# Performance work log

Hardware: AMD Instinct MI355X
Metric: run time of the kernel (lower is better)

The kernel has to match this reference:

```python
import jax, jax.numpy as jnp
import numpy as np

NODES_PER_GRAPH = 57
NUM_BRANCHES = 80
NUM_GRAPHS = 4096
IN_CH = 4
HID = 128
NUM_LAYERS = 5
BN_EPS = 1e-5


def setup_inputs() -> dict:
    key = jax.random.key(0)
    ks = jax.random.split(key, 24)
    N = NUM_GRAPHS * NODES_PER_GRAPH
    E = NUM_GRAPHS * NUM_BRANCHES * 2  # bidirectional branches per graph
    x = jax.random.normal(ks[0], (N, IN_CH), dtype=jnp.float32)
    # within-graph random edges, offset per graph block
    ep = jax.random.randint(ks[1], (2, E), 0, NODES_PER_GRAPH, dtype=jnp.int32)
    off = jnp.repeat(jnp.arange(NUM_GRAPHS, dtype=jnp.int32) * NODES_PER_GRAPH,
                     NUM_BRANCHES * 2)
    edge_index = ep + off[None, :]
    i = np.arange(NUM_BRANCHES)
    branch_u = jnp.asarray(i % NODES_PER_GRAPH, dtype=jnp.int32)
    branch_v = jnp.asarray((i * 7 + 3) % NODES_PER_GRAPH, dtype=jnp.int32)
    s = 0.05
    return {
        "x": x, "edge_index": edge_index,
        "branch_u": branch_u, "branch_v": branch_v,
        "Wp": jax.random.normal(ks[2], (IN_CH, HID)) * s,
        "bp": jnp.zeros((HID,), jnp.float32),
        "conv_W": jax.random.normal(ks[3], (NUM_LAYERS, HID, HID)) * s,
        "conv_b": jnp.zeros((NUM_LAYERS, HID), jnp.float32),
        "bn_gamma": jnp.ones((NUM_LAYERS, HID), jnp.float32),
        "bn_beta": jnp.zeros((NUM_LAYERS, HID), jnp.float32),
        "bn_mean": jax.random.normal(ks[4], (NUM_LAYERS, HID)) * 0.1,
        "bn_var": jax.random.uniform(ks[5], (NUM_LAYERS, HID)) + 0.5,
        "phys_W1": jax.random.normal(ks[6], (HID, 16)) * s,
        "phys_b1": jnp.zeros((16,), jnp.float32),
        "phys_W2": jax.random.normal(ks[7], (16, 1)) * s,
        "phys_b2": jnp.zeros((1,), jnp.float32),
        "mlp_W1": jax.random.normal(ks[8], (2 * HID + 1, HID)) * s,
        "mlp_b1": jnp.zeros((HID,), jnp.float32),
        "mlp_W2": jax.random.normal(ks[9], (HID, 1)) * s,
        "mlp_b2": jnp.zeros((1,), jnp.float32),
    }


def _gcn_conv(x, edge_index, W, b, num_nodes):
    # PyG GCNConv: add self-loops, symmetric deg^{-1/2} normalization,
    # message = norm * (x @ W)[src], scatter-add into dst, then + bias.
    h = x @ W
    loop = jnp.arange(num_nodes, dtype=edge_index.dtype)
    src = jnp.concatenate([edge_index[0], loop])
    dst = jnp.concatenate([edge_index[1], loop])
    deg = jax.ops.segment_sum(jnp.ones_like(dst, dtype=h.dtype), dst,
                              num_segments=num_nodes)  # >= 1 (self-loop)
    dinv = jax.lax.rsqrt(deg)
    norm = dinv[src] * dinv[dst]  # [E+N]
    out = jax.ops.segment_sum(h[src] * norm[:, None], dst,
                              num_segments=num_nodes)
    return out + b


def _forward(x, edge_index, branch_u, branch_v, Wp, bp, conv_W, conv_b,
             bn_gamma, bn_beta, bn_mean, bn_var, phys_W1, phys_b1, phys_W2,
             phys_b2, mlp_W1, mlp_b1, mlp_W2, mlp_b2):
    N = x.shape[0]
    num_graphs = N // NODES_PER_GRAPH
    h = x @ Wp + bp
    for l in range(NUM_LAYERS):
        res = h
        h = _gcn_conv(h, edge_index, conv_W[l], conv_b[l], N)
        # BatchNorm1d in eval mode (running stats); dropout is identity in eval
        h = (h - bn_mean[l]) * jax.lax.rsqrt(bn_var[l] + BN_EPS) * bn_gamma[l] + bn_beta[l]
        h = jax.nn.relu(h)
        h = h + res
    theta = jax.nn.relu(h @ phys_W1 + phys_b1) @ phys_W2 + phys_b2  # [N,1]
    offsets = (jnp.arange(num_graphs, dtype=jnp.int32) * NODES_PER_GRAPH)
    u_idx = (branch_u[None, :] + offsets[:, None]).reshape(-1)
    v_idx = (branch_v[None, :] + offsets[:, None]).reshape(-1)
    edge_feat = jnp.concatenate([h[u_idx], h[v_idx]], axis=-1)  # [G*80, 2H]
    delta_theta = theta[u_idx] - theta[v_idx]                   # [G*80, 1]
    comb = jnp.concatenate([edge_feat, delta_theta], axis=-1)
    return jax.nn.relu(comb @ mlp_W1 + mlp_b1) @ mlp_W2 + mlp_b2


def reference(x, edge_index, branch_u, branch_v, Wp, bp, conv_W, conv_b,
              bn_gamma, bn_beta, bn_mean, bn_var, phys_W1, phys_b1, phys_W2,
              phys_b2, mlp_W1, mlp_b1, mlp_W2, mlp_b2):
    return _forward(x, edge_index, branch_u, branch_v, Wp, bp, conv_W, conv_b,
                    bn_gamma, bn_beta, bn_mean, bn_var, phys_W1, phys_b1,
                    phys_W2, phys_b2, mlp_W1, mlp_b1, mlp_W2, mlp_b2)
```

## Files before the change

### kernel.cpp

```cpp
#include <hip/hip_runtime.h>

#define NPG 57
#define NEPG 160
#define NB 80
#define HID 128
#define NG 4096
#define NL 5

typedef __attribute__((ext_vector_type(8))) short bf16x8;
typedef __attribute__((ext_vector_type(4))) float f32x4;

__device__ __forceinline__ short f2bf(float f) {
    unsigned u = __builtin_bit_cast(unsigned, f);
    u += 0x7fff + ((u >> 16) & 1);
    return (short)(u >> 16);
}
__device__ __forceinline__ float bf2f(short s) {
    unsigned u = ((unsigned)(unsigned short)s) << 16;
    return __builtin_bit_cast(float, u);
}

__device__ __forceinline__ void cvt_pack(float4 a, float4 b, bf16x8& h8, bf16x8& l8) {
#define CVT1(X, I) { short hj = f2bf(X); h8[I] = hj; l8[I] = f2bf((X) - bf2f(hj)); }
    CVT1(a.x, 0) CVT1(a.y, 1) CVT1(a.z, 2) CVT1(a.w, 3)
    CVT1(b.x, 4) CVT1(b.y, 5) CVT1(b.z, 6) CVT1(b.w, 7)
#undef CVT1
}

__device__ __forceinline__ void frag_ks(const float (*A)[HID], int row, int kb, int ks,
                                        bf16x8& fh, bf16x8& fl) {
    const int sw = (row & 7) << 2;
    const float* rp = A[row];
    float4 q0 = *(const float4*)&rp[(32 * ks + kb) ^ sw];
    float4 q1 = *(const float4*)&rp[(32 * ks + kb + 4) ^ sw];
    cvt_pack(q0, q1, fh, fl);
}

template<int NCT>
__device__ __forceinline__ void mm_ks(f32x4* acc, const bf16x8& fh, const bf16x8& fl,
                                      const short* __restrict__ whi,
                                      const short* __restrict__ wlo,
                                      int ln15, int kb, int ks, int ctbase) {
#pragma unroll
    for (int j = 0; j < NCT; ++j) {
        int ct = ctbase + j;
        bf16x8 bhi = *(const bf16x8*)(whi + (16 * ct + ln15) * HID + kb + 32 * ks);
        bf16x8 blo = *(const bf16x8*)(wlo + (16 * ct + ln15) * HID + kb + 32 * ks);
        f32x4 a = acc[j];
        a = __builtin_amdgcn_mfma_f32_16x16x32_bf16(fh, bhi, a, 0, 0, 0);
        a = __builtin_amdgcn_mfma_f32_16x16x32_bf16(fh, blo, a, 0, 0, 0);
        a = __builtin_amdgcn_mfma_f32_16x16x32_bf16(fl, bhi, a, 0, 0, 0);
        acc[j] = a;
    }
}

__global__ void prep(const float* __restrict__ convW, const float* __restrict__ mlpW1,
                     const float* __restrict__ physW1, const float* __restrict__ convb,
                     const float* __restrict__ bn_gamma, const float* __restrict__ bn_beta,
                     const float* __restrict__ bn_mean, const float* __restrict__ bn_var,
                     short* __restrict__ wb, float* __restrict__ fsc, float* __restrict__ fsh) {
    int id = blockIdx.x * 256 + threadIdx.x;
    if (id < 114688) {
        int mat = id >> 14, rem = id & 16383, n = rem >> 7, k = rem & 127;
        float w;
        if (mat < 5)       w = convW[mat * 16384 + k * 128 + n];
        else if (mat == 5) w = mlpW1[k * 128 + n];
        else               w = mlpW1[(128 + k) * 128 + n];
        short hi = f2bf(w);
        short lo = f2bf(w - bf2f(hi));
        wb[mat * 32768 + n * 128 + k] = hi;
        wb[mat * 32768 + 16384 + n * 128 + k] = lo;
    } else if (id < 116736) {
        int p = id - 114688, n = p >> 7, k = p & 127;
        float w = physW1[k * 16 + n];
        short hi = f2bf(w);
        short lo = f2bf(w - bf2f(hi));
        wb[229376 + p] = hi;
        wb[231424 + p] = lo;
    } else if (id < 117376) {
        int p = id - 116736;
        float sc = bn_gamma[p] * rsqrtf(bn_var[p] + 1e-5f);
        float sh = fmaf(convb[p] - bn_mean[p], sc, bn_beta[p]);
        fsc[p] = sc;
        fsh[p] = sh;
    }
}

__global__ __launch_bounds__(512, 2) void pinn_fused(
    const float* __restrict__ x, const int* __restrict__ edge_index,
    const int* __restrict__ branch_u, const int* __restrict__ branch_v,
    const float* __restrict__ Wp, const float* __restrict__ bp,
    const float* __restrict__ physb1, const float* __restrict__ physW2,
    const float* __restrict__ physb2,
    const float* __restrict__ mlpW1, const float* __restrict__ mlpb1,
    const float* __restrict__ mlpW2, const float* __restrict__ mlpb2,
    const short* __restrict__ wb, const float* __restrict__ fsc,
    const float* __restrict__ fsh, float* __restrict__ out) {
    __shared__ float h[64][HID];
    __shared__ float dinv[NPG];
    __shared__ int   deg[NPG];
    __shared__ int   rowptr[NPG + 1];
    __shared__ int   cursor[NPG];
    __shared__ short esrc[NEPG], edst[NEPG];
    __shared__ int2  csre[NEPG + NPG];
    __shared__ float theta[64];
    __shared__ float red[NB];
    __shared__ int   bu[NB], bv[NB];

    const int g = blockIdx.x;
    const int tid = threadIdx.x;
    const int lane = tid & 63;
    const int wv = tid >> 6;
    const int ln15 = lane & 15;
    const int hi4 = lane >> 4;
    const int kb = hi4 << 3;
    const int c = tid & 127;
    const int rg = tid >> 7;
    const int wrow = wv & 3;
    const int ctbase = (wv >> 2) * 4;
    const int row = 16 * wrow + ln15;
    const int r0 = 16 * wrow + 4 * hi4;

    {
        float w0 = Wp[c], w1 = Wp[HID + c], w2 = Wp[2 * HID + c], w3 = Wp[3 * HID + c];
        float bb = bp[c];
        for (int r = rg; r < NPG; r += 4) {
            float4 xv = ((const float4*)x)[g * NPG + r];
            h[r][c ^ ((r & 7) << 2)] =
                fmaf(xv.x, w0, fmaf(xv.y, w1, fmaf(xv.z, w2, fmaf(xv.w, w3, bb))));
        }
    }
    if (tid < NPG) deg[tid] = 1;
    if (tid < NB) { bu[tid] = branch_u[tid]; bv[tid] = branch_v[tid]; red[tid] = 0.f; }
    for (int i = tid; i < 7 * HID; i += 512) h[57 + (i >> 7)][i & 127] = 0.f;
    __syncthreads();

    if (tid < NEPG) {
        int gs = edge_index[g * NEPG + tid];
        int gd = edge_index[NG * NEPG + g * NEPG + tid];
        short ls = (short)(gs - g * NPG);
        short ld = (short)(gd - g * NPG);
        esrc[tid] = ls;
        edst[tid] = ld;
        atomicAdd(&deg[ld], 1);
    }
    __syncthreads();

    if (wv == 0) {
        int dv = (lane < NPG) ? deg[lane] : 0;
        if (lane < NPG) dinv[lane] = rsqrtf((float)dv);
        int val = dv;
#pragma unroll
        for (int o = 1; o < 64; o <<= 1) {
            int t = __shfl_up(val, o, 64);
            if (lane >= o) val += t;
        }
        if (lane < NPG) { rowptr[lane + 1] = val; cursor[lane] = val - dv; }
        if (lane == 0) rowptr[0] = 0;
    }
    __syncthreads();

    if (tid < NEPG) {
        int s = esrc[tid], d = edst[tid];
        int pos = atomicAdd(&cursor[d], 1);
        csre[pos] = make_int2(s, __builtin_bit_cast(int, dinv[s] * dinv[d]));
    }
    if (tid < NPG) {
        int pos = atomicAdd(&cursor[tid], 1);
        csre[pos] = make_int2(tid, __builtin_bit_cast(int, dinv[tid] * dinv[tid]));
    }
    __syncthreads();

    for (int l = 0; l < NL; ++l) {
        const short* whi = wb + 2 * l * 16384;
        const short* wlo = wb + (2 * l + 1) * 16384;
        const int e0 = (row < NPG) ? rowptr[row] : 0;
        const int e1 = (row < NPG) ? rowptr[row + 1] : 0;

        f32x4 acc[4];
#pragma unroll
        for (int j = 0; j < 4; ++j) acc[j] = (f32x4){0.f, 0.f, 0.f, 0.f};

#pragma unroll
        for (int ks = 0; ks < 4; ++ks) {
            float4 pa = {0.f, 0.f, 0.f, 0.f};
            float4 qa = {0.f, 0.f, 0.f, 0.f};
            for (int e = e0; e < e1; ++e) {
                int2 ce = csre[e];
                const float* hp = h[ce.x];
                float w = __builtin_bit_cast(float, ce.y);
                const int sw = (ce.x & 7) << 2;
                float4 p0 = *(const float4*)&hp[(32 * ks + kb) ^ sw];
                float4 p1 = *(const float4*)&hp[(32 * ks + kb + 4) ^ sw];
                pa.x = fmaf(w, p0.x, pa.x); pa.y = fmaf(w, p0.y, pa.y);
                pa.z = fmaf(w, p0.z, pa.z); pa.w = fmaf(w, p0.w, pa.w);
                qa.x = fmaf(w, p1.x, qa.x); qa.y = fmaf(w, p1.y, qa.y);
                qa.z = fmaf(w, p1.z, qa.z); qa.w = fmaf(w, p1.w, qa.w);
            }
            bf16x8 fh, fl;
            cvt_pack(pa, qa, fh, fl);
            mm_ks<4>(acc, fh, fl, whi, wlo, ln15, kb, ks, ctbase);
        }
        __syncthreads();

        const float* sc = fsc + l * HID;
        const float* sh = fsh + l * HID;
#pragma unroll
        for (int j = 0; j < 4; ++j) {
            int ch = 16 * (ctbase + j) + ln15;
            float scv = sc[ch], shv = sh[ch];
#pragma unroll
            for (int q = 0; q < 4; ++q) {
                int rr = r0 + q;
                if (rr < NPG) {
                    float v = fmaf(acc[j][q], scv, shv);
                    int idx = ch ^ ((rr & 7) << 2);
                    h[rr][idx] = fmaxf(v, 0.f) + h[rr][idx];
                }
            }
        }
        __syncthreads();
    }

    if (wv < 4) {
        f32x4 t4 = (f32x4){0.f, 0.f, 0.f, 0.f};
#pragma unroll
        for (int ks = 0; ks < 4; ++ks) {
            bf16x8 fh, fl;
            frag_ks(h, row, kb, ks, fh, fl);
            mm_ks<1>(&t4, fh, fl, wb + 229376, wb + 231424, ln15, kb, ks, 0);
        }
        float b1 = physb1[ln15], w2 = physW2[ln15], b2 = physb2[0];
#pragma unroll
        for (int q = 0; q < 4; ++q) {
            float val = fmaxf(t4[q] + b1, 0.f) * w2;
#pragma unroll
            for (int o = 1; o < 16; o <<= 1) val += __shfl_xor(val, o, 16);
            if (ln15 == 0 && r0 + q < NPG) theta[r0 + q] = val + b2;
        }
    }
    __syncthreads();

    for (int task = wv; task < 10; task += 8) {
        int t = task >> 1;
        int cb = (task & 1) * 4;
        int b = 16 * t + ln15;
        int ru = bu[b], rv = bv[b];
        f32x4 acc[4];
#pragma unroll
        for (int j = 0; j < 4; ++j) acc[j] = (f32x4){0.f, 0.f, 0.f, 0.f};
#pragma unroll
        for (int ks = 0; ks < 4; ++ks) {
            bf16x8 fh, fl;
            frag_ks(h, ru, kb, ks, fh, fl);
            mm_ks<4>(acc, fh, fl, wb + 10 * 16384, wb + 11 * 16384, ln15, kb, ks, cb);
            frag_ks(h, rv, kb, ks, fh, fl);
            mm_ks<4>(acc, fh, fl, wb + 12 * 16384, wb + 13 * 16384, ln15, kb, ks, cb);
        }

        float dth[4];
#pragma unroll
        for (int q = 0; q < 4; ++q) {
            int bb = 16 * t + 4 * hi4 + q;
            dth[q] = theta[bu[bb]] - theta[bv[bb]];
        }
        float sums[4] = {0.f, 0.f, 0.f, 0.f};
#pragma unroll
        for (int j = 0; j < 4; ++j) {
            int ch = 16 * (cb + j) + ln15;
            float w256 = mlpW1[256 * HID + ch];
            float b1 = mlpb1[ch];
            float w2 = mlpW2[ch];
#pragma unroll
            for (int q = 0; q < 4; ++q) {
                float val = fmaxf(fmaf(dth[q], w256, acc[j][q] + b1), 0.f) * w2;
                sums[q] += val;
            }
        }
#pragma unroll
        for (int q = 0; q < 4; ++q) {
#pragma unroll
            for (int o = 1; o < 16; o <<= 1) sums[q] += __shfl_xor(sums[q], o, 16);
            if (ln15 == 0) atomicAdd(&red[16 * t + 4 * hi4 + q], sums[q]);
        }
    }
    __syncthreads();
    if (tid < NB) out[g * NB + tid] = red[tid] + mlpb2[0];
}

extern "C" void kernel_launch(void* const* d_in, const int* in_sizes, int n_in,
                              void* d_out, int out_size, void* d_ws, size_t ws_size,
                              hipStream_t stream) {
    const float* x          = (const float*)d_in[0];
    const int*   edge_index = (const int*)d_in[1];
    const int*   branch_u   = (const int*)d_in[2];
    const int*   branch_v   = (const int*)d_in[3];
    const float* Wp         = (const float*)d_in[4];
    const float* bp         = (const float*)d_in[5];
    const float* convW      = (const float*)d_in[6];
    const float* convb      = (const float*)d_in[7];
    const float* bn_gamma   = (const float*)d_in[8];
    const float* bn_beta    = (const float*)d_in[9];
    const float* bn_mean    = (const float*)d_in[10];
    const float* bn_var     = (const float*)d_in[11];
    const float* physW1     = (const float*)d_in[12];
    const float* physb1     = (const float*)d_in[13];
    const float* physW2     = (const float*)d_in[14];
    const float* physb2     = (const float*)d_in[15];
    const float* mlpW1      = (const float*)d_in[16];
    const float* mlpb1      = (const float*)d_in[17];
    const float* mlpW2      = (const float*)d_in[18];
    const float* mlpb2      = (const float*)d_in[19];
    float* out = (float*)d_out;

    short* wb = (short*)d_ws;
    float* fsc = (float*)((char*)d_ws + 466944);
    float* fsh = fsc + 640;

    prep<<<459, 256, 0, stream>>>(convW, mlpW1, physW1, convb,
                                  bn_gamma, bn_beta, bn_mean, bn_var, wb, fsc, fsh);
    pinn_fused<<<NG, 512, 0, stream>>>(
        x, edge_index, branch_u, branch_v, Wp, bp,
        physb1, physW2, physb2, mlpW1, mlpb1, mlpW2, mlpb2,
        wb, fsc, fsh, out);
}
```

Before: 1.073 ms.

## Replace CSR sparse aggregation with dense adjacency MFMA and packed hi/lo storage

```diff
diff --git a/kernel.cpp b/kernel.cpp
--- a/kernel.cpp
+++ b/kernel.cpp
@@ -9,31 +9,45 @@
 
 typedef __attribute__((ext_vector_type(8))) short bf16x8;
 typedef __attribute__((ext_vector_type(4))) float f32x4;
+typedef unsigned int u32;
 
 __device__ __forceinline__ short f2bf(float f) {
-    unsigned u = __builtin_bit_cast(unsigned, f);
+    u32 u = __builtin_bit_cast(u32, f);
     u += 0x7fff + ((u >> 16) & 1);
     return (short)(u >> 16);
 }
 __device__ __forceinline__ float bf2f(short s) {
-    unsigned u = ((unsigned)(unsigned short)s) << 16;
+    u32 u = ((u32)(unsigned short)s) << 16;
     return __builtin_bit_cast(float, u);
 }
-
-__device__ __forceinline__ void cvt_pack(float4 a, float4 b, bf16x8& h8, bf16x8& l8) {
-#define CVT1(X, I) { short hj = f2bf(X); h8[I] = hj; l8[I] = f2bf((X) - bf2f(hj)); }
-    CVT1(a.x, 0) CVT1(a.y, 1) CVT1(a.z, 2) CVT1(a.w, 3)
-    CVT1(b.x, 4) CVT1(b.y, 5) CVT1(b.z, 6) CVT1(b.w, 7)
-#undef CVT1
-}
-
-__device__ __forceinline__ void frag_ks(const float (*A)[HID], int row, int kb, int ks,
+__device__ __forceinline__ u32 packhl(float v) {
+    short hi = f2bf(v);
+    short lo = f2bf(v - bf2f(hi));
+    return (((u32)(unsigned short)hi) << 16) | (u32)(unsigned short)lo;
+}
+__device__ __forceinline__ float unpackf(u32 u) {
+    return bf2f((short)(u >> 16)) + bf2f((short)(u & 0xFFFFu));
+}
+
+__device__ __forceinline__ void unpack_frag(uint4 a, uint4 b, bf16x8& fh, bf16x8& fl) {
+    uint4 h, l;
+    h.x = (a.y & 0xFFFF0000u) | (a.x >> 16);
+    h.y = (a.w & 0xFFFF0000u) | (a.z >> 16);
+    h.z = (b.y & 0xFFFF0000u) | (b.x >> 16);
+    h.w = (b.w & 0xFFFF0000u) | (b.z >> 16);
+    l.x = (a.y << 16) | (a.x & 0xFFFFu);
+    l.y = (a.w << 16) | (a.z & 0xFFFFu);
+    l.z = (b.y << 16) | (b.x & 0xFFFFu);
+    l.w = (b.w << 16) | (b.z & 0xFFFFu);
+    fh = __builtin_bit_cast(bf16x8, h);
+    fl = __builtin_bit_cast(bf16x8, l);
+}
+
+__device__ __forceinline__ void frag_pk(const u32* rowp, int k0, int sw,
                                         bf16x8& fh, bf16x8& fl) {
-    const int sw = (row & 7) << 2;
-    const float* rp = A[row];
-    float4 q0 = *(const float4*)&rp[(32 * ks + kb) ^ sw];
-    float4 q1 = *(const float4*)&rp[(32 * ks + kb + 4) ^ sw];
-    cvt_pack(q0, q1, fh, fl);
+    uint4 a = *(const uint4*)((const char*)rowp + ((k0 * 4) ^ sw));
+    uint4 b = *(const uint4*)((const char*)rowp + (((k0 + 4) * 4) ^ sw));
+    unpack_frag(a, b, fh, fl);
 }
 
 template<int NCT>
@@ -86,7 +100,7 @@
     }
 }
 
-__global__ __launch_bounds__(512, 2) void pinn_fused(
+__global__ __launch_bounds__(1024, 4) void pinn_fused(
     const float* __restrict__ x, const int* __restrict__ edge_index,
     const int* __restrict__ branch_u, const int* __restrict__ branch_v,
     const float* __restrict__ Wp, const float* __restrict__ bp,
@@ -96,13 +110,13 @@
     const float* __restrict__ mlpW2, const float* __restrict__ mlpb2,
     const short* __restrict__ wb, const float* __restrict__ fsc,
     const float* __restrict__ fsh, float* __restrict__ out) {
-    __shared__ float h[64][HID];
-    __shared__ float dinv[NPG];
-    __shared__ int   deg[NPG];
-    __shared__ int   rowptr[NPG + 1];
-    __shared__ int   cursor[NPG];
+    __shared__ u32  hTu[128][64];
+    __shared__ u32  pool[64 * 128];
+    __shared__ short Ahi[64 * 64];
+    __shared__ short Alo[64 * 64];
+    __shared__ float dinv[64];
+    __shared__ int   deg[64];
     __shared__ short esrc[NEPG], edst[NEPG];
-    __shared__ int2  csre[NEPG + NPG];
     __shared__ float theta[64];
     __shared__ float red[NB];
     __shared__ int   bu[NB], bv[NB];
@@ -114,109 +128,129 @@
     const int ln15 = lane & 15;
     const int hi4 = lane >> 4;
     const int kb = hi4 << 3;
-    const int c = tid & 127;
-    const int rg = tid >> 7;
-    const int wrow = wv & 3;
-    const int ctbase = (wv >> 2) * 4;
-    const int row = 16 * wrow + ln15;
-    const int r0 = 16 * wrow + 4 * hi4;
+    const int R0 = 16 * (wv & 3);
+    const int ct0 = 2 * (wv >> 2);
 
     {
-        float w0 = Wp[c], w1 = Wp[HID + c], w2 = Wp[2 * HID + c], w3 = Wp[3 * HID + c];
-        float bb = bp[c];
-        for (int r = rg; r < NPG; r += 4) {
-            float4 xv = ((const float4*)x)[g * NPG + r];
-            h[r][c ^ ((r & 7) << 2)] =
-                fmaf(xv.x, w0, fmaf(xv.y, w1, fmaf(xv.z, w2, fmaf(xv.w, w3, bb))));
-        }
-    }
-    if (tid < NPG) deg[tid] = 1;
+        int r = lane;
+        float4 xv = make_float4(0.f, 0.f, 0.f, 0.f);
+        if (r < NPG) xv = ((const float4*)x)[g * NPG + r];
+        for (int c = 8 * wv; c < 8 * wv + 8; ++c) {
+            float h0 = 0.f;
+            if (r < NPG)
+                h0 = fmaf(xv.x, Wp[c], fmaf(xv.y, Wp[HID + c],
+                     fmaf(xv.z, Wp[2 * HID + c], fmaf(xv.w, Wp[3 * HID + c], bp[c]))));
+            *(u32*)((char*)&hTu[c][0] + ((r * 4) ^ ((c & 7) << 4))) = packhl(h0);
+        }
+    }
+    if (tid < 64) deg[tid] = (tid < NPG) ? 1 : 0;
     if (tid < NB) { bu[tid] = branch_u[tid]; bv[tid] = branch_v[tid]; red[tid] = 0.f; }
-    for (int i = tid; i < 7 * HID; i += 512) h[57 + (i >> 7)][i & 127] = 0.f;
+    {
+        float* Af = (float*)pool;
+        for (int i = tid; i < 4096; i += 1024) Af[i] = 0.f;
+    }
     __syncthreads();
 
     if (tid < NEPG) {
         int gs = edge_index[g * NEPG + tid];
         int gd = edge_index[NG * NEPG + g * NEPG + tid];
-        short ls = (short)(gs - g * NPG);
-        short ld = (short)(gd - g * NPG);
-        esrc[tid] = ls;
-        edst[tid] = ld;
-        atomicAdd(&deg[ld], 1);
-    }
-    __syncthreads();
-
-    if (wv == 0) {
-        int dv = (lane < NPG) ? deg[lane] : 0;
-        if (lane < NPG) dinv[lane] = rsqrtf((float)dv);
-        int val = dv;
-#pragma unroll
-        for (int o = 1; o < 64; o <<= 1) {
-            int t = __shfl_up(val, o, 64);
-            if (lane >= o) val += t;
-        }
-        if (lane < NPG) { rowptr[lane + 1] = val; cursor[lane] = val - dv; }
-        if (lane == 0) rowptr[0] = 0;
-    }
-    __syncthreads();
-
-    if (tid < NEPG) {
-        int s = esrc[tid], d = edst[tid];
-        int pos = atomicAdd(&cursor[d], 1);
-        csre[pos] = make_int2(s, __builtin_bit_cast(int, dinv[s] * dinv[d]));
-    }
-    if (tid < NPG) {
-        int pos = atomicAdd(&cursor[tid], 1);
-        csre[pos] = make_int2(tid, __builtin_bit_cast(int, dinv[tid] * dinv[tid]));
-    }
-    __syncthreads();
-
+        esrc[tid] = (short)(gs - g * NPG);
+        edst[tid] = (short)(gd - g * NPG);
+        atomicAdd(&deg[edst[tid]], 1);
+    }
+    __syncthreads();
+    if (tid < 64) dinv[tid] = (tid < NPG) ? rsqrtf((float)deg[tid]) : 0.f;
+    __syncthreads();
+    {
+        float* Af = (float*)pool;
+        if (tid < NEPG) {
+            int s = esrc[tid], d = edst[tid];
+            atomicAdd(&Af[d * 64 + s], dinv[s] * dinv[d]);
+        }
+        if (tid < NPG) atomicAdd(&Af[tid * 64 + tid], dinv[tid] * dinv[tid]);
+    }
+    __syncthreads();
+    {
+        const float* Af = (const float*)pool;
+        for (int i = tid; i < 4096; i += 1024) {
+            float a = Af[i];
+            short hi = f2bf(a);
+            Ahi[i] = hi;
+            Alo[i] = f2bf(a - bf2f(hi));
+        }
+    }
+    __syncthreads();
+
+    bf16x8 afh[2], afl[2];
+#pragma unroll
+    for (int ks2 = 0; ks2 < 2; ++ks2) {
+        int off = (R0 + ln15) * 64 + 32 * ks2 + kb;
+        afh[ks2] = *(const bf16x8*)&Ahi[off];
+        afl[ks2] = *(const bf16x8*)&Alo[off];
+    }
+
+    u32* mpk = pool;
     for (int l = 0; l < NL; ++l) {
+        f32x4 acc[2];
+        acc[0] = (f32x4){0.f, 0.f, 0.f, 0.f};
+        acc[1] = (f32x4){0.f, 0.f, 0.f, 0.f};
+#pragma unroll
+        for (int ks2 = 0; ks2 < 2; ++ks2) {
+#pragma unroll
+            for (int j = 0; j < 2; ++j) {
+                int c = 16 * (ct0 + j) + ln15;
+                bf16x8 hh, hl;
+                frag_pk(&hTu[c][0], 32 * ks2 + kb, (c & 7) << 4, hh, hl);
+                f32x4 a = acc[j];
+                a = __builtin_amdgcn_mfma_f32_16x16x32_bf16(afh[ks2], hh, a, 0, 0, 0);
+                a = __builtin_amdgcn_mfma_f32_16x16x32_bf16(afh[ks2], hl, a, 0, 0, 0);
+                a = __builtin_amdgcn_mfma_f32_16x16x32_bf16(afl[ks2], hh, a, 0, 0, 0);
+                acc[j] = a;
+            }
+        }
+#pragma unroll
+        for (int j = 0; j < 2; ++j) {
+#pragma unroll
+            for (int q = 0; q < 4; ++q) {
+                int rr = R0 + 4 * hi4 + q;
+                int cc = 16 * (ct0 + j) + ln15;
+                *(u32*)((char*)&mpk[rr * 128] + ((cc * 4) ^ ((rr & 7) << 4))) =
+                    packhl(acc[j][q]);
+            }
+        }
+        __syncthreads();
+
+        f32x4 z2[2];
+        z2[0] = (f32x4){0.f, 0.f, 0.f, 0.f};
+        z2[1] = (f32x4){0.f, 0.f, 0.f, 0.f};
         const short* whi = wb + 2 * l * 16384;
         const short* wlo = wb + (2 * l + 1) * 16384;
-        const int e0 = (row < NPG) ? rowptr[row] : 0;
-        const int e1 = (row < NPG) ? rowptr[row + 1] : 0;
-
-        f32x4 acc[4];
-#pragma unroll
-        for (int j = 0; j < 4; ++j) acc[j] = (f32x4){0.f, 0.f, 0.f, 0.f};
-
 #pragma unroll
         for (int ks = 0; ks < 4; ++ks) {
-            float4 pa = {0.f, 0.f, 0.f, 0.f};
-            float4 qa = {0.f, 0.f, 0.f, 0.f};
-            for (int e = e0; e < e1; ++e) {
-                int2 ce = csre[e];
-                const float* hp = h[ce.x];
-                float w = __builtin_bit_cast(float, ce.y);
-                const int sw = (ce.x & 7) << 2;
-                float4 p0 = *(const float4*)&hp[(32 * ks + kb) ^ sw];
-                float4 p1 = *(const float4*)&hp[(32 * ks + kb + 4) ^ sw];
-                pa.x = fmaf(w, p0.x, pa.x); pa.y = fmaf(w, p0.y, pa.y);
-                pa.z = fmaf(w, p0.z, pa.z); pa.w = fmaf(w, p0.w, pa.w);
-                qa.x = fmaf(w, p1.x, qa.x); qa.y = fmaf(w, p1.y, qa.y);
-                qa.z = fmaf(w, p1.z, qa.z); qa.w = fmaf(w, p1.w, qa.w);
-            }
-            bf16x8 fh, fl;
-            cvt_pack(pa, qa, fh, fl);
-            mm_ks<4>(acc, fh, fl, whi, wlo, ln15, kb, ks, ctbase);
-        }
-        __syncthreads();
+            bf16x8 mh, ml;
+            int rr = R0 + ln15;
+            frag_pk(&mpk[rr * 128], 32 * ks + kb, (rr & 7) << 4, mh, ml);
+            mm_ks<2>(z2, mh, ml, whi, wlo, ln15, kb, ks, ct0);
+        }
+        if (l == NL - 1) __syncthreads();
 
         const float* sc = fsc + l * HID;
         const float* sh = fsh + l * HID;
 #pragma unroll
-        for (int j = 0; j < 4; ++j) {
-            int ch = 16 * (ctbase + j) + ln15;
-            float scv = sc[ch], shv = sh[ch];
+        for (int j = 0; j < 2; ++j) {
+            int cc = 16 * (ct0 + j) + ln15;
+            float scv = sc[cc], shv = sh[cc];
 #pragma unroll
             for (int q = 0; q < 4; ++q) {
-                int rr = r0 + q;
-                if (rr < NPG) {
-                    float v = fmaf(acc[j][q], scv, shv);
-                    int idx = ch ^ ((rr & 7) << 2);
-                    h[rr][idx] = fmaxf(v, 0.f) + h[rr][idx];
-                }
+                int rr = R0 + 4 * hi4 + q;
+                u32* hp = (u32*)((char*)&hTu[cc][0] + ((rr * 4) ^ ((cc & 7) << 4)));
+                float hold = unpackf(*hp);
+                float hnew = fmaxf(fmaf(z2[j][q], scv, shv), 0.f) + hold;
+                if (l == NL - 1)
+                    *(u32*)((char*)&pool[rr * 128] + ((cc * 4) ^ ((rr & 7) << 4))) =
+                        packhl(hnew);
+                else
+                    *hp = packhl(hnew);
             }
         }
         __syncthreads();
@@ -224,11 +258,16 @@
 
     if (wv < 4) {
         f32x4 t4 = (f32x4){0.f, 0.f, 0.f, 0.f};
+        int r = 16 * wv + ln15;
 #pragma unroll
         for (int ks = 0; ks < 4; ++ks) {
             bf16x8 fh, fl;
-            frag_ks(h, row, kb, ks, fh, fl);
-            mm_ks<1>(&t4, fh, fl, wb + 229376, wb + 231424, ln15, kb, ks, 0);
+            frag_pk(&pool[r * 128], 32 * ks + kb, (r & 7) << 4, fh, fl);
+            bf16x8 bh = *(const bf16x8*)(wb + 229376 + ln15 * HID + 32 * ks + kb);
+            bf16x8 bl = *(const bf16x8*)(wb + 231424 + ln15 * HID + 32 * ks + kb);
+            t4 = __builtin_amdgcn_mfma_f32_16x16x32_bf16(fh, bh, t4, 0, 0, 0);
+            t4 = __builtin_amdgcn_mfma_f32_16x16x32_bf16(fh, bl, t4, 0, 0, 0);
+            t4 = __builtin_amdgcn_mfma_f32_16x16x32_bf16(fl, bh, t4, 0, 0, 0);
         }
         float b1 = physb1[ln15], w2 = physW2[ln15], b2 = physb2[0];
 #pragma unroll
@@ -236,28 +275,28 @@
             float val = fmaxf(t4[q] + b1, 0.f) * w2;
 #pragma unroll
             for (int o = 1; o < 16; o <<= 1) val += __shfl_xor(val, o, 16);
-            if (ln15 == 0 && r0 + q < NPG) theta[r0 + q] = val + b2;
-        }
-    }
-    __syncthreads();
-
-    for (int task = wv; task < 10; task += 8) {
+            int rq = 16 * wv + 4 * hi4 + q;
+            if (ln15 == 0 && rq < NPG) theta[rq] = val + b2;
+        }
+    }
+    __syncthreads();
+
+    for (int task = wv; task < 10; task += 16) {
         int t = task >> 1;
         int cb = (task & 1) * 4;
         int b = 16 * t + ln15;
         int ru = bu[b], rv = bv[b];
-        f32x4 acc[4];
-#pragma unroll
-        for (int j = 0; j < 4; ++j) acc[j] = (f32x4){0.f, 0.f, 0.f, 0.f};
+        f32x4 acc4[4];
+#pragma unroll
+        for (int j = 0; j < 4; ++j) acc4[j] = (f32x4){0.f, 0.f, 0.f, 0.f};
 #pragma unroll
         for (int ks = 0; ks < 4; ++ks) {
             bf16x8 fh, fl;
-            frag_ks(h, ru, kb, ks, fh, fl);
-            mm_ks<4>(acc, fh, fl, wb + 10 * 16384, wb + 11 * 16384, ln15, kb, ks, cb);
-            frag_ks(h, rv, kb, ks, fh, fl);
-            mm_ks<4>(acc, fh, fl, wb + 12 * 16384, wb + 13 * 16384, ln15, kb, ks, cb);
-        }
-
+            frag_pk(&pool[ru * 128], 32 * ks + kb, (ru & 7) << 4, fh, fl);
+            mm_ks<4>(acc4, fh, fl, wb + 10 * 16384, wb + 11 * 16384, ln15, kb, ks, cb);
+            frag_pk(&pool[rv * 128], 32 * ks + kb, (rv & 7) << 4, fh, fl);
+            mm_ks<4>(acc4, fh, fl, wb + 12 * 16384, wb + 13 * 16384, ln15, kb, ks, cb);
+        }
         float dth[4];
 #pragma unroll
         for (int q = 0; q < 4; ++q) {
@@ -272,10 +311,8 @@
             float b1 = mlpb1[ch];
             float w2 = mlpW2[ch];
 #pragma unroll
-            for (int q = 0; q < 4; ++q) {
-                float val = fmaxf(fmaf(dth[q], w256, acc[j][q] + b1), 0.f) * w2;
-                sums[q] += val;
-            }
+            for (int q = 0; q < 4; ++q)
+                sums[q] += fmaxf(fmaf(dth[q], w256, acc4[j][q] + b1), 0.f) * w2;
         }
 #pragma unroll
         for (int q = 0; q < 4; ++q) {
@@ -319,7 +356,7 @@
 
     prep<<<459, 256, 0, stream>>>(convW, mlpW1, physW1, convb,
                                   bn_gamma, bn_beta, bn_mean, bn_var, wb, fsc, fsh);
-    pinn_fused<<<NG, 512, 0, stream>>>(
+    pinn_fused<<<NG, 1024, 0, stream>>>(
         x, edge_index, branch_u, branch_v, Wp, bp,
         physb1, physW2, physb2, mlpW1, mlpb1, mlpW2, mlpb2,
         wb, fsc, fsh, out);
```

Result: slower. 1.221 ms (+13.8%).
